# Kernel optimization log

Hardware: AMD Instinct MI355X
Metric: run time of the kernel (lower is better)

## Reference

```python
import jax, jax.numpy as jnp
import numpy as np


def setup_inputs() -> dict:
    key = jax.random.key(0)
    kx, ky = jax.random.split(key)
    B, N, M, D = 4, 8192, 8192, 3
    x = jax.random.normal(kx, (B, N, D), dtype=jnp.float32)
    y = jax.random.normal(ky, (B, M, D), dtype=jnp.float32)
    return {"x": x, "y": y}


def reference(x, y):
    # Pairwise squared distances: [B, N, M]
    x2 = jnp.sum(x * x, axis=-1)  # [B, N]
    y2 = jnp.sum(y * y, axis=-1)  # [B, M]
    xy = jnp.einsum("bnd,bmd->bnm", x, y)  # [B, N, M]
    d2 = x2[:, :, None] + y2[:, None, :] - 2.0 * xy
    # Chamfer: min over the other set in each direction
    min_xy = jnp.min(d2, axis=2)  # [B, N] nearest y for each x
    min_yx = jnp.min(d2, axis=1)  # [B, M] nearest x for each y
    return jnp.mean(min_xy) + jnp.mean(min_yx)
```

## Files before the change

### kernel.cpp

```cpp
#include <hip/hip_runtime.h>

#define BATCHES 4
#define NPTS    8192
#define INF32   3.0e38f

typedef _Float16 f16x8  __attribute__((ext_vector_type(8)));
typedef float    f32x16 __attribute__((ext_vector_type(16)));

__device__ inline void fsplit(float v, _Float16& h, _Float16& l) {
    h = (_Float16)v;
    l = (_Float16)(v - (float)h);
}

__device__ inline void pack_point(float p0, float p1, float p2,
                                  _Float16* __restrict__ avec,
                                  _Float16* __restrict__ bvec)
{
    _Float16 h[3], l[3];
    fsplit(p0, h[0], l[0]); fsplit(p1, h[1], l[1]); fsplit(p2, h[2], l[2]);
    float q = fmaf(p2, p2, fmaf(p1, p1, p0 * p0));
    _Float16 qh, ql;
    fsplit(q, qh, ql);

    __align__(16) _Float16 av[16];
    __align__(16) _Float16 bv[16];
    #pragma unroll
    for (int k = 0; k < 3; ++k) {
        av[k]     = h[k];
        av[3 + k] = l[k];
        av[6 + k] = h[k];
        bv[k]     = (_Float16)(-2.0f * (float)h[k]);
        bv[3 + k] = bv[k];
        bv[6 + k] = (_Float16)(-2.0f * (float)l[k]);
    }
    av[9] = qh; av[10] = ql; av[11] = (_Float16)1.0f; av[12] = (_Float16)1.0f;
    bv[9] = (_Float16)1.0f; bv[10] = (_Float16)1.0f; bv[11] = qh; bv[12] = ql;
    av[13] = av[14] = av[15] = (_Float16)0.0f;
    bv[13] = bv[14] = bv[15] = (_Float16)0.0f;

    ((int4*)avec)[0] = ((int4*)av)[0]; ((int4*)avec)[1] = ((int4*)av)[1];
    ((int4*)bvec)[0] = ((int4*)bv)[0]; ((int4*)bvec)[1] = ((int4*)bv)[1];
}

__global__ __launch_bounds__(256) void chamfer_prep(
    const float* __restrict__ x, const float* __restrict__ y,
    _Float16* __restrict__ pAx, _Float16* __restrict__ pBx,
    _Float16* __restrict__ pAy, _Float16* __restrict__ pBy,
    int* __restrict__ mininit )
{
    int i = blockIdx.x * 256 + threadIdx.x;
    mininit[i]         = 0x7F7F7F7F;
    mininit[i + 32768] = 0x7F7F7F7F;

    const float* xp = x + (size_t)i * 3;
    const float* yp = y + (size_t)i * 3;
    pack_point(xp[0], xp[1], xp[2], pAx + (size_t)i * 16, pBx + (size_t)i * 16);
    pack_point(yp[0], yp[1], yp[2], pAy + (size_t)i * 16, pBy + (size_t)i * 16);
}

__global__ __launch_bounds__(256, 4) void chamfer_mfma(
    const _Float16* __restrict__ pAx, const _Float16* __restrict__ pBx,
    const _Float16* __restrict__ pAy, const _Float16* __restrict__ pBy,
    float* __restrict__ minall )
{
    int bid      = blockIdx.x;
    int dir      = bid >> 10;
    int b        = (bid >> 8) & 3;
    int rowstrip = (bid >> 2) & 63;
    int colchunk = bid & 3;
    int tid      = threadIdx.x;
    int wv       = tid >> 6, lane = tid & 63;
    int lo       = lane & 31, hi = lane >> 5;

    const _Float16* Adata = ((dir == 0) ? pAx : pAy) + (size_t)b * NPTS * 16;
    const _Float16* Bdata = ((dir == 0) ? pBy : pBx) + (size_t)b * NPTS * 16;
    float* outMin = minall + ((size_t)dir << 15) + (size_t)b * NPTS;

    int rw = rowstrip * 128 + wv * 32;
    int c0 = colchunk * 2048;

    f16x8 af = *(const f16x8*)(Adata + ((size_t)(rw + lo) << 4) + (hi << 3));

    float rmin[16];
    #pragma unroll
    for (int r = 0; r < 16; ++r) rmin[r] = INF32;

    const f32x16 zero = {0.f,0.f,0.f,0.f,0.f,0.f,0.f,0.f,
                         0.f,0.f,0.f,0.f,0.f,0.f,0.f,0.f};

    auto loadB = [&](int t) -> f16x8 {
        return *(const f16x8*)(Bdata + ((size_t)(c0 + (t << 5) + lo) << 4) + (hi << 3));
    };

#define MIN3X16(P0, P1)                                                \
    _Pragma("unroll")                                                  \
    for (int r = 0; r < 16; ++r)                                       \
        rmin[r] = fminf(fminf(P0[r], P1[r]), rmin[r]);

    f16x8 bcA0 = loadB(0), bcA1 = loadB(1);
    f32x16 accA0 = __builtin_amdgcn_mfma_f32_32x32x16_f16(af, bcA0, zero, 0, 0, 0);
    f32x16 accA1 = __builtin_amdgcn_mfma_f32_32x32x16_f16(af, bcA1, zero, 0, 0, 0);
    f16x8 bcB0 = loadB(2), bcB1 = loadB(3);
    f32x16 accB0, accB1;

    #pragma unroll 1
    for (int q = 0; q < 15; ++q) {
        accB0 = __builtin_amdgcn_mfma_f32_32x32x16_f16(af, bcB0, zero, 0, 0, 0);
        accB1 = __builtin_amdgcn_mfma_f32_32x32x16_f16(af, bcB1, zero, 0, 0, 0);
        bcA0 = loadB(4 * q + 4); bcA1 = loadB(4 * q + 5);
        MIN3X16(accA0, accA1)
        accA0 = __builtin_amdgcn_mfma_f32_32x32x16_f16(af, bcA0, zero, 0, 0, 0);
        accA1 = __builtin_amdgcn_mfma_f32_32x32x16_f16(af, bcA1, zero, 0, 0, 0);
        bcB0 = loadB(4 * q + 6); bcB1 = loadB(4 * q + 7);
        MIN3X16(accB0, accB1)
    }
    accB0 = __builtin_amdgcn_mfma_f32_32x32x16_f16(af, bcB0, zero, 0, 0, 0);
    accB1 = __builtin_amdgcn_mfma_f32_32x32x16_f16(af, bcB1, zero, 0, 0, 0);
    MIN3X16(accA0, accA1)
    MIN3X16(accB0, accB1)
#undef MIN3X16

    #pragma unroll
    for (int r = 0; r < 16; ++r) {
        float v = rmin[r];
        v = fminf(v, __shfl_xor(v, 1, 64));
        v = fminf(v, __shfl_xor(v, 2, 64));
        v = fminf(v, __shfl_xor(v, 4, 64));
        v = fminf(v, __shfl_xor(v, 8, 64));
        v = fminf(v, __shfl_xor(v, 16, 64));
        if (lo == 0) {
            int rr = (r & 3) + ((r >> 2) << 3) + (hi << 2);
            atomicMin((int*)&outMin[rw + rr], __float_as_int(fmaxf(v, 0.f)));
        }
    }
}

__global__ __launch_bounds__(1024) void chamfer_reduce(
    const float* __restrict__ minbuf, float* __restrict__ out)
{
    int tid = threadIdx.x;
    double s = 0.0;
    #pragma unroll
    for (int q = 0; q < 16; ++q) {
        float4 v = *reinterpret_cast<const float4*>(minbuf + (q * 1024 + tid) * 4);
        s += ((double)v.x + (double)v.y) + ((double)v.z + (double)v.w);
    }
    #pragma unroll
    for (int off = 32; off > 0; off >>= 1) s += __shfl_down(s, off, 64);
    __shared__ double sd[16];
    if ((tid & 63) == 0) sd[tid >> 6] = s;
    __syncthreads();
    if (tid == 0) {
        double t = 0.0;
        #pragma unroll
        for (int w = 0; w < 16; ++w) t += sd[w];
        out[0] = (float)(t / (double)(BATCHES * NPTS));
    }
}

extern "C" void kernel_launch(void* const* d_in, const int* in_sizes, int n_in,
                              void* d_out, int out_size, void* d_ws, size_t ws_size,
                              hipStream_t stream)
{
    const float* x = (const float*)d_in[0];
    const float* y = (const float*)d_in[1];
    float* out = (float*)d_out;

    float*    minall = (float*)d_ws;
    _Float16* pAx = (_Float16*)(minall + 65536);
    _Float16* pBx = pAx + (size_t)BATCHES * NPTS * 16;
    _Float16* pAy = pBx + (size_t)BATCHES * NPTS * 16;
    _Float16* pBy = pAy + (size_t)BATCHES * NPTS * 16;

    chamfer_prep<<<BATCHES * NPTS / 256, 256, 0, stream>>>(
        x, y, pAx, pBx, pAy, pBy, (int*)minall);
    chamfer_mfma<<<2048, 256, 0, stream>>>(pAx, pBx, pAy, pBy, minall);
    chamfer_reduce<<<1, 1024, 0, stream>>>(minall, out);
}
```

Baseline: 40.07 us.

## Compute both chamfer directions from one distance matrix pass

Each block now computes the x-to-y distance tile once and takes both row minima and column minima from it, instead of launching a second set of blocks for the y-to-x direction. Column minima are folded in registers, combined across the half-waves with a shuffle, staged in a 32 KB shared buffer per block, merged across waves, and written with atomicMin. This halves the MFMA work and the grid size. In exchange, every tile now carries extra min/shuffle/LDS-store work, plus a sync and 2048 extra global atomics per block, and the shared buffer may lower occupancy.

```diff
diff --git a/kernel.cpp b/kernel.cpp
--- a/kernel.cpp
+++ b/kernel.cpp
@@ -12,72 +12,72 @@
     l = (_Float16)(v - (float)h);
 }
 
-__device__ inline void pack_point(float p0, float p1, float p2,
-                                  _Float16* __restrict__ avec,
-                                  _Float16* __restrict__ bvec)
-{
-    _Float16 h[3], l[3];
-    fsplit(p0, h[0], l[0]); fsplit(p1, h[1], l[1]); fsplit(p2, h[2], l[2]);
-    float q = fmaf(p2, p2, fmaf(p1, p1, p0 * p0));
-    _Float16 qh, ql;
-    fsplit(q, qh, ql);
-
-    __align__(16) _Float16 av[16];
-    __align__(16) _Float16 bv[16];
-    #pragma unroll
-    for (int k = 0; k < 3; ++k) {
-        av[k]     = h[k];
-        av[3 + k] = l[k];
-        av[6 + k] = h[k];
-        bv[k]     = (_Float16)(-2.0f * (float)h[k]);
-        bv[3 + k] = bv[k];
-        bv[6 + k] = (_Float16)(-2.0f * (float)l[k]);
-    }
-    av[9] = qh; av[10] = ql; av[11] = (_Float16)1.0f; av[12] = (_Float16)1.0f;
-    bv[9] = (_Float16)1.0f; bv[10] = (_Float16)1.0f; bv[11] = qh; bv[12] = ql;
-    av[13] = av[14] = av[15] = (_Float16)0.0f;
-    bv[13] = bv[14] = bv[15] = (_Float16)0.0f;
-
-    ((int4*)avec)[0] = ((int4*)av)[0]; ((int4*)avec)[1] = ((int4*)av)[1];
-    ((int4*)bvec)[0] = ((int4*)bv)[0]; ((int4*)bvec)[1] = ((int4*)bv)[1];
-}
-
 __global__ __launch_bounds__(256) void chamfer_prep(
     const float* __restrict__ x, const float* __restrict__ y,
-    _Float16* __restrict__ pAx, _Float16* __restrict__ pBx,
-    _Float16* __restrict__ pAy, _Float16* __restrict__ pBy,
+    _Float16* __restrict__ pA, _Float16* __restrict__ pB,
     int* __restrict__ mininit )
 {
     int i = blockIdx.x * 256 + threadIdx.x;
     mininit[i]         = 0x7F7F7F7F;
     mininit[i + 32768] = 0x7F7F7F7F;
 
-    const float* xp = x + (size_t)i * 3;
-    const float* yp = y + (size_t)i * 3;
-    pack_point(xp[0], xp[1], xp[2], pAx + (size_t)i * 16, pBx + (size_t)i * 16);
-    pack_point(yp[0], yp[1], yp[2], pAy + (size_t)i * 16, pBy + (size_t)i * 16);
+    {
+        const float* xp = x + (size_t)i * 3;
+        float p0 = xp[0], p1 = xp[1], p2 = xp[2];
+        _Float16 h[3], l[3];
+        fsplit(p0, h[0], l[0]); fsplit(p1, h[1], l[1]); fsplit(p2, h[2], l[2]);
+        float q = fmaf(p2, p2, fmaf(p1, p1, p0 * p0));
+        _Float16 qh, ql; fsplit(q, qh, ql);
+        __align__(16) _Float16 av[16];
+        #pragma unroll
+        for (int k = 0; k < 3; ++k) { av[k] = h[k]; av[3+k] = l[k]; av[6+k] = h[k]; }
+        av[9] = qh; av[10] = ql; av[11] = (_Float16)1.0f; av[12] = (_Float16)1.0f;
+        av[13] = av[14] = av[15] = (_Float16)0.0f;
+        int4* dA = (int4*)(pA + (size_t)i * 16);
+        dA[0] = ((int4*)av)[0]; dA[1] = ((int4*)av)[1];
+    }
+    {
+        const float* yp = y + (size_t)i * 3;
+        float p0 = yp[0], p1 = yp[1], p2 = yp[2];
+        _Float16 h[3], l[3];
+        fsplit(p0, h[0], l[0]); fsplit(p1, h[1], l[1]); fsplit(p2, h[2], l[2]);
+        float s = fmaf(p2, p2, fmaf(p1, p1, p0 * p0));
+        _Float16 sh, sl; fsplit(s, sh, sl);
+        __align__(16) _Float16 bv[16];
+        #pragma unroll
+        for (int k = 0; k < 3; ++k) {
+            bv[k]     = (_Float16)(-2.0f * (float)h[k]);
+            bv[3 + k] = bv[k];
+            bv[6 + k] = (_Float16)(-2.0f * (float)l[k]);
+        }
+        bv[9] = (_Float16)1.0f; bv[10] = (_Float16)1.0f; bv[11] = sh; bv[12] = sl;
+        bv[13] = bv[14] = bv[15] = (_Float16)0.0f;
+        int4* dB = (int4*)(pB + (size_t)i * 16);
+        dB[0] = ((int4*)bv)[0]; dB[1] = ((int4*)bv)[1];
+    }
 }
 
 __global__ __launch_bounds__(256, 4) void chamfer_mfma(
-    const _Float16* __restrict__ pAx, const _Float16* __restrict__ pBx,
-    const _Float16* __restrict__ pAy, const _Float16* __restrict__ pBy,
+    const _Float16* __restrict__ pA, const _Float16* __restrict__ pB,
     float* __restrict__ minall )
 {
     int bid      = blockIdx.x;
-    int dir      = bid >> 10;
-    int b        = (bid >> 8) & 3;
+    int b        = bid >> 8;
     int rowstrip = (bid >> 2) & 63;
     int colchunk = bid & 3;
     int tid      = threadIdx.x;
     int wv       = tid >> 6, lane = tid & 63;
     int lo       = lane & 31, hi = lane >> 5;
 
-    const _Float16* Adata = ((dir == 0) ? pAx : pAy) + (size_t)b * NPTS * 16;
-    const _Float16* Bdata = ((dir == 0) ? pBy : pBx) + (size_t)b * NPTS * 16;
-    float* outMin = minall + ((size_t)dir << 15) + (size_t)b * NPTS;
+    const _Float16* Adata = pA + (size_t)b * NPTS * 16;
+    const _Float16* Bdata = pB + (size_t)b * NPTS * 16;
+    float* rowMin = minall + (size_t)b * NPTS;
+    float* colMin = minall + 32768 + (size_t)b * NPTS;
 
     int rw = rowstrip * 128 + wv * 32;
     int c0 = colchunk * 2048;
+
+    __shared__ float cmin[4][2048];
 
     f16x8 af = *(const f16x8*)(Adata + ((size_t)(rw + lo) << 4) + (hi << 3));
 
@@ -91,11 +91,28 @@
     auto loadB = [&](int t) -> f16x8 {
         return *(const f16x8*)(Bdata + ((size_t)(c0 + (t << 5) + lo) << 4) + (hi << 3));
     };
+
+    float* cbase = &cmin[wv][lo];
 
 #define MIN3X16(P0, P1)                                                \
     _Pragma("unroll")                                                  \
     for (int r = 0; r < 16; ++r)                                       \
         rmin[r] = fminf(fminf(P0[r], P1[r]), rmin[r]);
+
+#define COLFOLD(P, T)                                                  \
+    {                                                                  \
+        float m0 = fminf(fminf(P[0],  P[1]),  P[2]);                   \
+        float m1 = fminf(fminf(P[3],  P[4]),  P[5]);                   \
+        float m2 = fminf(fminf(P[6],  P[7]),  P[8]);                   \
+        float m3 = fminf(fminf(P[9],  P[10]), P[11]);                  \
+        float m4 = fminf(fminf(P[12], P[13]), P[14]);                  \
+        float m5 = fminf(fminf(m0, m1), P[15]);                        \
+        float m6 = fminf(fminf(m2, m3), m4);                           \
+        float cv = fminf(m5, m6);                                      \
+        cv = fminf(cv, __shfl_xor(cv, 32, 64));                        \
+        cv = fmaxf(cv, 0.f);                                           \
+        if (hi == 0) cbase[(T) << 5] = cv;                             \
+    }
 
     f16x8 bcA0 = loadB(0), bcA1 = loadB(1);
     f32x16 accA0 = __builtin_amdgcn_mfma_f32_32x32x16_f16(af, bcA0, zero, 0, 0, 0);
@@ -109,16 +126,25 @@
         accB1 = __builtin_amdgcn_mfma_f32_32x32x16_f16(af, bcB1, zero, 0, 0, 0);
         bcA0 = loadB(4 * q + 4); bcA1 = loadB(4 * q + 5);
         MIN3X16(accA0, accA1)
+        COLFOLD(accA0, 4 * q)
+        COLFOLD(accA1, 4 * q + 1)
         accA0 = __builtin_amdgcn_mfma_f32_32x32x16_f16(af, bcA0, zero, 0, 0, 0);
         accA1 = __builtin_amdgcn_mfma_f32_32x32x16_f16(af, bcA1, zero, 0, 0, 0);
         bcB0 = loadB(4 * q + 6); bcB1 = loadB(4 * q + 7);
         MIN3X16(accB0, accB1)
+        COLFOLD(accB0, 4 * q + 2)
+        COLFOLD(accB1, 4 * q + 3)
     }
     accB0 = __builtin_amdgcn_mfma_f32_32x32x16_f16(af, bcB0, zero, 0, 0, 0);
     accB1 = __builtin_amdgcn_mfma_f32_32x32x16_f16(af, bcB1, zero, 0, 0, 0);
     MIN3X16(accA0, accA1)
+    COLFOLD(accA0, 60)
+    COLFOLD(accA1, 61)
     MIN3X16(accB0, accB1)
+    COLFOLD(accB0, 62)
+    COLFOLD(accB1, 63)
 #undef MIN3X16
+#undef COLFOLD
 
     #pragma unroll
     for (int r = 0; r < 16; ++r) {
@@ -130,8 +156,17 @@
         v = fminf(v, __shfl_xor(v, 16, 64));
         if (lo == 0) {
             int rr = (r & 3) + ((r >> 2) << 3) + (hi << 2);
-            atomicMin((int*)&outMin[rw + rr], __float_as_int(fmaxf(v, 0.f)));
+            atomicMin((int*)&rowMin[rw + rr], __float_as_int(fmaxf(v, 0.f)));
         }
+    }
+
+    __syncthreads();
+    #pragma unroll
+    for (int c = 0; c < 2048; c += 256) {
+        int cc = c + tid;
+        float m = fminf(fminf(cmin[0][cc], cmin[1][cc]),
+                        fminf(cmin[2][cc], cmin[3][cc]));
+        atomicMin((int*)&colMin[c0 + cc], __float_as_int(m));
     }
 }
 
@@ -167,13 +202,11 @@
     float* out = (float*)d_out;
 
     float*    minall = (float*)d_ws;
-    _Float16* pAx = (_Float16*)(minall + 65536);
-    _Float16* pBx = pAx + (size_t)BATCHES * NPTS * 16;
-    _Float16* pAy = pBx + (size_t)BATCHES * NPTS * 16;
-    _Float16* pBy = pAy + (size_t)BATCHES * NPTS * 16;
-
-    chamfer_prep<<<BATCHES * NPTS / 256, 256, 0, stream>>>(
-        x, y, pAx, pBx, pAy, pBy, (int*)minall);
-    chamfer_mfma<<<2048, 256, 0, stream>>>(pAx, pBx, pAy, pBy, minall);
+    _Float16* pA = (_Float16*)(minall + 65536);
+    _Float16* pB = pA + (size_t)BATCHES * NPTS * 16;
+
+    chamfer_prep<<<BATCHES * NPTS / 256, 256, 0, stream>>>(x, y, pA, pB,
+                                                           (int*)minall);
+    chamfer_mfma<<<1024, 256, 0, stream>>>(pA, pB, minall);
     chamfer_reduce<<<1, 1024, 0, stream>>>(minall, out);
 }
```

Measured after the change: 54.75 us. 36.6% more time.
